# Kernel tuning notes

Hardware: AMD Instinct MI355X
Metric: run time of the kernel (lower is better)

## Reference

```python
import jax, jax.numpy as jnp
import numpy as np


def _conv1x1(t, W, b):
    # 1x1 conv == per-pixel channel GEMM: [B,C,H,W] x [O,C] -> [B,O,H,W]
    return jnp.einsum('bchw,oc->bohw', t, W) + b[None, :, None, None]


def setup_inputs() -> dict:
    key = jax.random.key(0)
    ks = jax.random.split(key, 10)
    B, C, H, W = 8, 256, 96, 96
    s = 1.0 / np.sqrt(C)
    inp = {
        'x': jax.random.normal(ks[0], (B, C, H, W), dtype=jnp.float32),
        'Wq': jax.random.normal(ks[1], (C, C), dtype=jnp.float32) * s,
        'bq': jax.random.normal(ks[2], (C,), dtype=jnp.float32) * 0.01,
        'Wk': jax.random.normal(ks[3], (C, C), dtype=jnp.float32) * s,
        'bk': jax.random.normal(ks[4], (C,), dtype=jnp.float32) * 0.01,
        'Wv': jax.random.normal(ks[5], (C, C), dtype=jnp.float32) * s,
        'bv': jax.random.normal(ks[6], (C,), dtype=jnp.float32) * 0.01,
        'Ws': jax.random.normal(ks[7], (C, C), dtype=jnp.float32) * s,
        'bs': jax.random.normal(ks[8], (C,), dtype=jnp.float32) * 0.01,
        # torch init is zeros; use a nonzero scalar so the attention branch matters
        'gamma': jax.random.normal(ks[9], (1,), dtype=jnp.float32) * 0.5,
    }
    return inp


def reference(x, Wq, bq, Wk, bk, Wv, bv, Ws, bs, gamma):
    B, C, H, W = x.shape
    N = H * W
    # query: [B, N, C]
    q = _conv1x1(x, Wq, bq).reshape(B, C, N).transpose(0, 2, 1)
    # key: 1x1 conv, then stride-3 1x1 conv (== subsample every 3rd pixel, then GEMM)
    k = _conv1x1(x, Wk, bk)
    k = _conv1x1(k[:, :, ::3, ::3], Ws, bs)
    Ns = k.shape[2] * k.shape[3]
    k = k.reshape(B, C, Ns)
    energy = jnp.einsum('bnc,bcm->bnm', q, k)       # [B, N, Ns]
    attn = jax.nn.softmax(energy, axis=-1)
    # value: same 1x1 conv + strided 1x1 conv pipeline
    v = _conv1x1(x, Wv, bv)
    v = _conv1x1(v[:, :, ::3, ::3], Ws, bs).reshape(B, C, Ns)
    out = jnp.einsum('bcm,bnm->bcn', v, attn).reshape(B, C, H, W)
    return gamma[0] * out + x
```

## Files before the change

### kernel.cpp

```cpp
#include <hip/hip_runtime.h>

typedef _Float16 f16;
typedef _Float16 f16x8 __attribute__((ext_vector_type(8)));
typedef __fp16 fp16x2 __attribute__((ext_vector_type(2)));
typedef float f32x4 __attribute__((ext_vector_type(4)));
typedef float f32x16 __attribute__((ext_vector_type(16)));

#define CDIM 256
#define NPIX 9216
#define NB 8

__device__ __forceinline__ f32x4 mfma16(f16x8 a, f16x8 b, f32x4 c) {
  return __builtin_amdgcn_mfma_f32_16x16x32_f16(a, b, c, 0, 0, 0);
}
__device__ __forceinline__ f32x16 mfma32(f16x8 a, f16x8 b, f32x16 c) {
  return __builtin_amdgcn_mfma_f32_32x32x16_f16(a, b, c, 0, 0, 0);
}
__device__ __forceinline__ f16x8 ld8(const f16* p) { return *(const f16x8*)p; }

__device__ __forceinline__ void stage16(const void* g, void* l) {
  __builtin_amdgcn_global_load_lds((const __attribute__((address_space(1))) unsigned int*)g,
                                   (__attribute__((address_space(3))) unsigned int*)l, 16, 0, 0);
}
#define S_BARRIER() do { asm volatile("" ::: "memory"); __builtin_amdgcn_s_barrier(); asm volatile("" ::: "memory"); } while (0)
#define WAIT_VM(N) do { asm volatile("s_waitcnt vmcnt(" #N ")" ::: "memory"); __builtin_amdgcn_sched_barrier(0); } while (0)

__device__ __forceinline__ unsigned pkrtz(float a, float b) {
  union { fp16x2 h; unsigned u; } cv;
  cv.h = __builtin_amdgcn_cvt_pkrtz(a, b);
  return cv.u;
}
union U8 { f16x8 v; unsigned u[4]; };

__device__ __forceinline__ f16x8 pack_swap(float v0, float v1, float v2, float v3,
                                           float v4, float v5, float v6, float v7,
                                           int hh) {
  unsigned a  = pkrtz(v0, v1);
  unsigned b2 = pkrtz(v2, v3);
  unsigned c2 = pkrtz(v4, v5);
  unsigned d2 = pkrtz(v6, v7);
  unsigned ex1 = __shfl_xor(hh ? a : c2, 32);
  unsigned ex2 = __shfl_xor(hh ? b2 : d2, 32);
  U8 r;
  r.u[0] = hh ? ex1 : a;
  r.u[1] = hh ? ex2 : b2;
  r.u[2] = hh ? c2 : ex1;
  r.u[3] = hh ? d2 : ex2;
  return r.v;
}


__global__ void prep_weights(const float* __restrict__ Wq,
                             const float* __restrict__ Wk, const float* __restrict__ bk,
                             const float* __restrict__ Wv, const float* __restrict__ bv,
                             const float* __restrict__ Ws, const float* __restrict__ bs,
                             f16* __restrict__ WqF, f16* __restrict__ Wk2H, f16* __restrict__ Wv2H,
                             float* __restrict__ bk2, float* __restrict__ bv2) {
  int o = blockIdx.x, c = threadIdx.x;
  float ak = 0.f, av = 0.f;
  for (int i = 0; i < CDIM; ++i) {
    float w = Ws[o*CDIM + i];
    ak += w * Wk[i*CDIM + c];
    av += w * Wv[i*CDIM + c];
  }
  Wk2H[o*CDIM + c] = (f16)ak;
  Wv2H[o*CDIM + c] = (f16)av;
  {
    size_t byte = (size_t)((o >> 5)*16 + (c >> 4))*1024
                + (size_t)(((c >> 3) & 1)*32 + (o & 31))*16 + (c & 7)*2;
    *(f16*)((char*)WqF + byte) = (f16)Wq[o*CDIM + c];
  }
  if (c == 0) {
    float sk = 0.f, sv = 0.f;
    for (int i = 0; i < CDIM; ++i) { float w = Ws[o*CDIM + i]; sk += w*bk[i]; sv += w*bv[i]; }
    bk2[o] = sk + bs[o];
    bv2[o] = sv + bs[o];
  }
}

__global__ void transpose_x(const float* __restrict__ x, char* __restrict__ xT) {
  __shared__ f16 tile[32][34];
  int c0 = blockIdx.x * 32, n0 = blockIdx.y * 32, b = blockIdx.z;
  int tx = threadIdx.x, ty = threadIdx.y;
#pragma unroll
  for (int j = 0; j < 4; ++j) {
    int cl = ty + 8*j;
    tile[cl][tx] = (f16)x[(size_t)(b*CDIM + c0 + cl)*NPIX + n0 + tx];
  }
  __syncthreads();
  int tid = ty*32 + tx;
  if (tid < 128) {
    int nl = tid >> 2, u = tid & 3;
    int n = n0 + nl;
    int cu = (c0 >> 3) + u;
    f16x8 v;
#pragma unroll
    for (int e = 0; e < 8; ++e) v[e] = tile[8*u + e][nl];
    size_t byte = (size_t)(b*NPIX + n)*512 + (size_t)((cu ^ (n & 7)) << 4);
    *(f16x8*)(xT + byte) = v;
  }
}

__global__ __launch_bounds__(256) void compute_kv(
    const char* __restrict__ xT, const f16* __restrict__ Wk2H, const f16* __restrict__ Wv2H,
    const float* __restrict__ bk2, const float* __restrict__ bv2,
    char* __restrict__ kB, char* __restrict__ vB) {
  int ch = blockIdx.x;
  int m0 = ch * 32;
  int b = blockIdx.y;
  int tid = threadIdx.x;
  int w = tid >> 6, lane = tid & 63, l15 = lane & 15, q = lane >> 4;
  size_t chbase = (size_t)(b*32 + ch)*16384;

  const char* xrow[2]; int xn7[2];
#pragma unroll
  for (int mt2 = 0; mt2 < 2; ++mt2) {
    int m = m0 + 16*mt2 + l15;
    int n = 288*(m >> 5) + 3*(m & 31);
    xrow[mt2] = xT + (size_t)(b*NPIX + n)*512;
    xn7[mt2] = n & 7;
  }
  const f16 *kwb[4], *vwb[4];
#pragma unroll
  for (int t = 0; t < 4; ++t) {
    kwb[t] = Wk2H + (size_t)(64*w + 16*t + l15)*CDIM + 8*q;
    vwb[t] = Wv2H + (size_t)(64*w + 16*t + l15)*CDIM + 8*q;
  }
  f32x4 accK[2][4] = {};
  f32x4 accV[4][2] = {};
  for (int ks = 0; ks < 8; ++ks) {
    f16x8 am[2], wk[4], wv[4];
#pragma unroll
    for (int mt2 = 0; mt2 < 2; ++mt2)
      am[mt2] = *(const f16x8*)(xrow[mt2] + (((q + 4*ks) ^ xn7[mt2]) << 4));
#pragma unroll
    for (int t = 0; t < 4; ++t) { wk[t] = ld8(kwb[t] + 32*ks); wv[t] = ld8(vwb[t] + 32*ks); }
#pragma unroll
    for (int mt2 = 0; mt2 < 2; ++mt2)
#pragma unroll
      for (int ot = 0; ot < 4; ++ot) {
        accK[mt2][ot] = mfma16(am[mt2], wk[ot], accK[mt2][ot]);
        accV[ot][mt2] = mfma16(wv[ot], am[mt2], accV[ot][mt2]);
      }
  }
#pragma unroll
  for (int mt2 = 0; mt2 < 2; ++mt2)
#pragma unroll
    for (int ot = 0; ot < 4; ++ot) {
      int cin = 64*w + 16*ot + l15;
      float bo = bk2[cin];
      size_t fb = chbase + (size_t)(cin >> 4)*1024 + (size_t)(((cin >> 3) & 1)*32)*16 + (cin & 7)*2;
#pragma unroll
      for (int r = 0; r < 4; ++r) {
        int keyrel = 16*mt2 + 4*q + r;
        *(f16*)(kB + fb + (size_t)keyrel*16) = (f16)(accK[mt2][ot][r] + bo);
      }
    }
#pragma unroll
  for (int ct = 0; ct < 4; ++ct) {
    f32x4 bv4 = *(const f32x4*)(bv2 + 64*w + 16*ct + 4*q);
#pragma unroll
    for (int mt2 = 0; mt2 < 2; ++mt2) {
#pragma unroll
      for (int r = 0; r < 4; ++r) {
        int c = 64*w + 16*ct + 4*q + r;
        size_t byte = chbase + (size_t)(2*(c >> 5) + mt2)*1024
                    + (size_t)((l15 >> 3)*32 + (c & 31))*16 + (l15 & 7)*2;
        *(f16*)(vB + byte) = (f16)(accV[ct][mt2][r] + bv4[r]);
      }
    }
  }
}

__global__ __launch_bounds__(256, 2) void attention(
    const char* __restrict__ xT, const f16* __restrict__ WqF, const float* __restrict__ bq,
    const char* __restrict__ kB, const char* __restrict__ vB,
    const float* __restrict__ xg, const float* __restrict__ gamma_p,
    float* __restrict__ out) {
  __shared__ char lds[65536];

  int bid = blockIdx.x;
  int b = bid & 7;
  int tile = bid >> 3;
  int tid = threadIdx.x;
  int w = tid >> 6, lane = tid & 63, l31 = lane & 31, hh = lane >> 5;
  int n0w = tile*128 + w*32;
  int lane16 = lane * 16;

  const char* kBb = kB + (size_t)b*524288;
  const char* vBb = vB + (size_t)b*524288;

  {
    int so = tid * 16;
#pragma unroll
    for (int r = 0; r < 4; ++r) stage16(kBb + so + r*4096, lds + so + r*4096);
#pragma unroll
    for (int r = 0; r < 4; ++r) stage16(vBb + so + r*4096, lds + 16384 + so + r*4096);
  }

  f16x8 qf[16];
  {
    f16x8 xb[16];
    int n = n0w + l31;
    const char* xrow = xT + (size_t)(b*NPIX + n)*512;
    int n7 = n & 7;
#pragma unroll
    for (int s = 0; s < 16; ++s)
      xb[s] = *(const f16x8*)(xrow + (((2*s + hh) ^ n7) << 4));
#pragma unroll
    for (int ot = 0; ot < 8; ++ot) {
      f32x16 acc;
#pragma unroll
      for (int j = 0; j < 16; ++j) acc[j] = 0.f;
#pragma unroll
      for (int s = 0; s < 16; ++s) {
        f16x8 wa = *(const f16x8*)((const char*)WqF + (size_t)(ot*16 + s)*1024 + lane16);
        acc = mfma32(wa, xb[s], acc);
      }
#pragma unroll
      for (int i = 0; i < 4; ++i) {
        f32x4 bv4 = *(const f32x4*)(bq + 32*ot + 8*i + 4*hh);
#pragma unroll
        for (int j2 = 0; j2 < 4; ++j2) acc[4*i + j2] += bv4[j2];
      }
      qf[2*ot + 0] = pack_swap(acc[0], acc[1], acc[2], acc[3],
                               acc[4], acc[5], acc[6], acc[7], hh);
      qf[2*ot + 1] = pack_swap(acc[8], acc[9], acc[10], acc[11],
                               acc[12], acc[13], acc[14], acc[15], hh);
    }
  }

  f32x16 O[8];
#pragma unroll
  for (int i = 0; i < 8; ++i)
#pragma unroll
    for (int j = 0; j < 16; ++j) O[i][j] = 0.f;
  float m_run = -3e38f, l_run = 0.f;

  for (int t = 0; t < 32; ++t) {
    char* curb = lds + ((t & 1) << 15);
    if (t < 31) {
      const char* ksrc = kBb + (size_t)(t + 1)*16384;
      const char* vsrc = vBb + (size_t)(t + 1)*16384;
      char* kd = lds + (((t + 1) & 1) << 15);
      int so = tid * 16;
#pragma unroll
      for (int r = 0; r < 4; ++r) stage16(ksrc + so + r*4096, kd + so + r*4096);
#pragma unroll
      for (int r = 0; r < 4; ++r) stage16(vsrc + so + r*4096, kd + 16384 + so + r*4096);
      WAIT_VM(8);
    } else {
      WAIT_VM(0);
    }
    S_BARRIER();

    f32x16 S16;
#pragma unroll
    for (int j = 0; j < 16; ++j) S16[j] = 0.f;
    __builtin_amdgcn_s_setprio(1);
#pragma unroll
    for (int s = 0; s < 16; ++s) {
      f16x8 kf = *(const f16x8*)(curb + s*1024 + lane16);
      S16 = mfma32(kf, qf[s], S16);
    }
    __builtin_amdgcn_s_setprio(0);

    float mx = S16[0];
#pragma unroll
    for (int j = 1; j < 16; ++j) mx = fmaxf(mx, S16[j]);
    mx = fmaxf(mx, __shfl_xor(mx, 32));
    if (!__all(mx <= m_run + 8.0f)) {
      float mn = fmaxf(m_run, mx);
      float al = __expf(m_run - mn);
      m_run = mn;
      l_run *= al;
#pragma unroll
      for (int i = 0; i < 8; ++i)
#pragma unroll
        for (int j = 0; j < 16; ++j) O[i][j] *= al;
    }
    float p[16];
    float ls = 0.f;
#pragma unroll
    for (int j = 0; j < 16; ++j) { p[j] = __expf(S16[j] - m_run); ls += p[j]; }
    l_run += ls;

    f16x8 pf0 = pack_swap(p[0], p[1], p[2], p[3], p[4], p[5], p[6], p[7], hh);
    f16x8 pf1 = pack_swap(p[8], p[9], p[10], p[11], p[12], p[13], p[14], p[15], hh);

    __builtin_amdgcn_s_setprio(1);
#pragma unroll
    for (int ct = 0; ct < 8; ++ct) {
      f16x8 vf0 = *(const f16x8*)(curb + 16384 + (ct*2 + 0)*1024 + lane16);
      O[ct] = mfma32(vf0, pf0, O[ct]);
      f16x8 vf1 = *(const f16x8*)(curb + 16384 + (ct*2 + 1)*1024 + lane16);
      O[ct] = mfma32(vf1, pf1, O[ct]);
    }
    __builtin_amdgcn_s_setprio(0);
    S_BARRIER();
  }

  l_run += __shfl_xor(l_run, 32);
  float inv = 1.0f / l_run;
  float g = gamma_p[0];
  int n = n0w + l31;
#pragma unroll
  for (int ct = 0; ct < 8; ++ct)
#pragma unroll
    for (int j = 0; j < 16; ++j) {
      int c = 32*ct + (j & 3) + 8*(j >> 2) + 4*hh;
      size_t idx = (size_t)(b*CDIM + c)*NPIX + n;
      out[idx] = g * (O[ct][j] * inv) + xg[idx];
    }
}

extern "C" void kernel_launch(void* const* d_in, const int* in_sizes, int n_in,
                              void* d_out, int out_size, void* d_ws, size_t ws_size,
                              hipStream_t stream) {
  (void)in_sizes; (void)n_in; (void)out_size; (void)ws_size;
  const float* x     = (const float*)d_in[0];
  const float* Wq    = (const float*)d_in[1];
  const float* bq    = (const float*)d_in[2];
  const float* Wk    = (const float*)d_in[3];
  const float* bk    = (const float*)d_in[4];
  const float* Wv    = (const float*)d_in[5];
  const float* bv    = (const float*)d_in[6];
  const float* Ws    = (const float*)d_in[7];
  const float* bs    = (const float*)d_in[8];
  const float* gamma = (const float*)d_in[9];

  char* ws = (char*)d_ws;
  float* bk2 = (float*)(ws);
  float* bv2 = (float*)(ws + 1024);
  char* xT   = ws + 4096;
  char* kB   = ws + 4096 + 37748736;
  char* vB   = kB + 4194304;
  f16* WqF   = (f16*)(vB + 4194304);
  f16* Wk2H  = WqF + 65536;
  f16* Wv2H  = Wk2H + 65536;

  prep_weights<<<256, 256, 0, stream>>>(Wq, Wk, bk, Wv, bv, Ws, bs, WqF, Wk2H, Wv2H, bk2, bv2);
  transpose_x<<<dim3(8, 288, 8), dim3(32, 8), 0, stream>>>(x, xT);
  compute_kv<<<dim3(32, 8), 256, 0, stream>>>(xT, Wk2H, Wv2H, bk2, bv2, kB, vB);
  attention<<<576, 256, 0, stream>>>(xT, WqF, bq, kB, vB, x, gamma, (float*)d_out);
}
```

Baseline: 197.2 us.

## Split attention warps into QK/softmax producers and PV consumers

Each block now handles 64 query pixels instead of 128. Two waves compute QK^T and the softmax and write the fp16 probabilities and rescale factors to LDS. The other two waves, one step behind, run the PV MFMAs and the final store. The grid doubles and K/V staging is offset so K for step t+1 and V for step t are loaded together. The goal is to overlap the softmax math with the PV matrix work, at the cost of extra LDS traffic, more LDS per block (about 73 KB) and half the pixels per block, which doubles the K/V reloads.

```diff
diff --git a/kernel.cpp b/kernel.cpp
--- a/kernel.cpp
+++ b/kernel.cpp
@@ -24,6 +24,7 @@
 }
 #define S_BARRIER() do { asm volatile("" ::: "memory"); __builtin_amdgcn_s_barrier(); asm volatile("" ::: "memory"); } while (0)
 #define WAIT_VM(N) do { asm volatile("s_waitcnt vmcnt(" #N ")" ::: "memory"); __builtin_amdgcn_sched_barrier(0); } while (0)
+#define WAIT_LGKM0() do { asm volatile("s_waitcnt lgkmcnt(0)" ::: "memory"); __builtin_amdgcn_sched_barrier(0); } while (0)
 
 __device__ __forceinline__ unsigned pkrtz(float a, float b) {
   union { fp16x2 h; unsigned u; } cv;
@@ -177,15 +178,22 @@
     const char* __restrict__ kB, const char* __restrict__ vB,
     const float* __restrict__ xg, const float* __restrict__ gamma_p,
     float* __restrict__ out) {
-  __shared__ char lds[65536];
+  __shared__ char lds[74496];
+  char* ldsK = lds;
+  char* ldsV = lds + 32768;
+  char* ldsP = lds + 65536;
+  float* ldsA = (float*)(lds + 73728);
+  float* ldsL = (float*)(lds + 74240);
 
   int bid = blockIdx.x;
   int b = bid & 7;
   int tile = bid >> 3;
   int tid = threadIdx.x;
   int w = tid >> 6, lane = tid & 63, l31 = lane & 31, hh = lane >> 5;
-  int n0w = tile*128 + w*32;
   int lane16 = lane * 16;
+  bool prod = (w < 2);
+  int rw = prod ? w : (w - 2);
+  int n0w = tile*64 + rw*32;
 
   const char* kBb = kB + (size_t)b*524288;
   const char* vBb = vB + (size_t)b*524288;
@@ -193,13 +201,11 @@
   {
     int so = tid * 16;
 #pragma unroll
-    for (int r = 0; r < 4; ++r) stage16(kBb + so + r*4096, lds + so + r*4096);
-#pragma unroll
-    for (int r = 0; r < 4; ++r) stage16(vBb + so + r*4096, lds + 16384 + so + r*4096);
+    for (int r = 0; r < 4; ++r) stage16(kBb + so + r*4096, ldsK + so + r*4096);
   }
 
   f16x8 qf[16];
-  {
+  if (prod) {
     f16x8 xb[16];
     int n = n0w + l31;
     const char* xrow = xT + (size_t)(b*NPIX + n)*512;
@@ -237,81 +243,122 @@
     for (int j = 0; j < 16; ++j) O[i][j] = 0.f;
   float m_run = -3e38f, l_run = 0.f;
 
-  for (int t = 0; t < 32; ++t) {
-    char* curb = lds + ((t & 1) << 15);
+  for (int t = 0; t <= 32; ++t) {
     if (t < 31) {
+      int so = tid * 16;
       const char* ksrc = kBb + (size_t)(t + 1)*16384;
-      const char* vsrc = vBb + (size_t)(t + 1)*16384;
-      char* kd = lds + (((t + 1) & 1) << 15);
+      char* kd = ldsK + ((t + 1) & 1)*16384;
+#pragma unroll
+      for (int r = 0; r < 4; ++r) stage16(ksrc + so + r*4096, kd + so + r*4096);
+      const char* vsrc = vBb + (size_t)t*16384;
+      char* vd = ldsV + (t & 1)*16384;
+#pragma unroll
+      for (int r = 0; r < 4; ++r) stage16(vsrc + so + r*4096, vd + so + r*4096);
+      WAIT_VM(8);
+    } else if (t == 31) {
       int so = tid * 16;
-#pragma unroll
-      for (int r = 0; r < 4; ++r) stage16(ksrc + so + r*4096, kd + so + r*4096);
-#pragma unroll
-      for (int r = 0; r < 4; ++r) stage16(vsrc + so + r*4096, kd + 16384 + so + r*4096);
-      WAIT_VM(8);
+      const char* vsrc = vBb + (size_t)31*16384;
+      char* vd = ldsV + (31 & 1)*16384;
+#pragma unroll
+      for (int r = 0; r < 4; ++r) stage16(vsrc + so + r*4096, vd + so + r*4096);
+      WAIT_VM(4);
     } else {
       WAIT_VM(0);
     }
     S_BARRIER();
 
-    f32x16 S16;
-#pragma unroll
-    for (int j = 0; j < 16; ++j) S16[j] = 0.f;
-    __builtin_amdgcn_s_setprio(1);
-#pragma unroll
-    for (int s = 0; s < 16; ++s) {
-      f16x8 kf = *(const f16x8*)(curb + s*1024 + lane16);
-      S16 = mfma32(kf, qf[s], S16);
-    }
-    __builtin_amdgcn_s_setprio(0);
-
-    float mx = S16[0];
-#pragma unroll
-    for (int j = 1; j < 16; ++j) mx = fmaxf(mx, S16[j]);
-    mx = fmaxf(mx, __shfl_xor(mx, 32));
-    if (!__all(mx <= m_run + 8.0f)) {
-      float mn = fmaxf(m_run, mx);
-      float al = __expf(m_run - mn);
-      m_run = mn;
-      l_run *= al;
-#pragma unroll
-      for (int i = 0; i < 8; ++i)
-#pragma unroll
-        for (int j = 0; j < 16; ++j) O[i][j] *= al;
-    }
-    float p[16];
-    float ls = 0.f;
-#pragma unroll
-    for (int j = 0; j < 16; ++j) { p[j] = __expf(S16[j] - m_run); ls += p[j]; }
-    l_run += ls;
-
-    f16x8 pf0 = pack_swap(p[0], p[1], p[2], p[3], p[4], p[5], p[6], p[7], hh);
-    f16x8 pf1 = pack_swap(p[8], p[9], p[10], p[11], p[12], p[13], p[14], p[15], hh);
-
-    __builtin_amdgcn_s_setprio(1);
-#pragma unroll
-    for (int ct = 0; ct < 8; ++ct) {
-      f16x8 vf0 = *(const f16x8*)(curb + 16384 + (ct*2 + 0)*1024 + lane16);
-      O[ct] = mfma32(vf0, pf0, O[ct]);
-      f16x8 vf1 = *(const f16x8*)(curb + 16384 + (ct*2 + 1)*1024 + lane16);
-      O[ct] = mfma32(vf1, pf1, O[ct]);
-    }
-    __builtin_amdgcn_s_setprio(0);
+    if (prod && t < 32) {
+      const char* kc = ldsK + (t & 1)*16384;
+      f32x16 SA, SB;
+#pragma unroll
+      for (int j = 0; j < 16; ++j) { SA[j] = 0.f; SB[j] = 0.f; }
+      __builtin_amdgcn_s_setprio(1);
+#pragma unroll
+      for (int s = 0; s < 8; ++s) {
+        f16x8 kfa = *(const f16x8*)(kc + (2*s)*1024 + lane16);
+        SA = mfma32(kfa, qf[2*s], SA);
+        f16x8 kfb = *(const f16x8*)(kc + (2*s + 1)*1024 + lane16);
+        SB = mfma32(kfb, qf[2*s + 1], SB);
+      }
+      __builtin_amdgcn_s_setprio(0);
+      f32x16 S16;
+#pragma unroll
+      for (int j = 0; j < 16; ++j) S16[j] = SA[j] + SB[j];
+
+      float mx = S16[0];
+#pragma unroll
+      for (int j = 1; j < 16; ++j) mx = fmaxf(mx, S16[j]);
+      mx = fmaxf(mx, __shfl_xor(mx, 32));
+      float al = 1.0f;
+      if (!__all(mx <= m_run + 8.0f)) {
+        float mn = fmaxf(m_run, mx);
+        al = __expf(m_run - mn);
+        m_run = mn;
+        l_run *= al;
+      }
+      float ls = 0.f;
+#pragma unroll
+      for (int j = 0; j < 16; ++j) { S16[j] = __expf(S16[j] - m_run); ls += S16[j]; }
+      l_run += ls;
+
+      f16x8 pf0 = pack_swap(S16[0], S16[1], S16[2], S16[3],
+                            S16[4], S16[5], S16[6], S16[7], hh);
+      f16x8 pf1 = pack_swap(S16[8], S16[9], S16[10], S16[11],
+                            S16[12], S16[13], S16[14], S16[15], hh);
+      char* pd = ldsP + (t & 1)*4096 + w*2048;
+      *(f16x8*)(pd + lane16) = pf0;
+      *(f16x8*)(pd + 1024 + lane16) = pf1;
+      if (lane < 32) ldsA[(t & 1)*64 + w*32 + l31] = al;
+    }
+
+    if (!prod && t >= 1) {
+      int tc = t - 1;
+      float al = ldsA[(tc & 1)*64 + rw*32 + l31];
+      if (!__all(al == 1.0f)) {
+#pragma unroll
+        for (int i = 0; i < 8; ++i)
+#pragma unroll
+          for (int j = 0; j < 16; ++j) O[i][j] *= al;
+      }
+      const char* pc = ldsP + (tc & 1)*4096 + rw*2048;
+      f16x8 pf0 = *(const f16x8*)(pc + lane16);
+      f16x8 pf1 = *(const f16x8*)(pc + 1024 + lane16);
+      const char* vc = ldsV + (tc & 1)*16384;
+      __builtin_amdgcn_s_setprio(1);
+#pragma unroll
+      for (int ct = 0; ct < 8; ++ct) {
+        f16x8 vf0 = *(const f16x8*)(vc + (ct*2 + 0)*1024 + lane16);
+        O[ct] = mfma32(vf0, pf0, O[ct]);
+        f16x8 vf1 = *(const f16x8*)(vc + (ct*2 + 1)*1024 + lane16);
+        O[ct] = mfma32(vf1, pf1, O[ct]);
+      }
+      __builtin_amdgcn_s_setprio(0);
+    }
+
+    WAIT_LGKM0();
     S_BARRIER();
   }
 
-  l_run += __shfl_xor(l_run, 32);
-  float inv = 1.0f / l_run;
-  float g = gamma_p[0];
-  int n = n0w + l31;
-#pragma unroll
-  for (int ct = 0; ct < 8; ++ct)
-#pragma unroll
-    for (int j = 0; j < 16; ++j) {
-      int c = 32*ct + (j & 3) + 8*(j >> 2) + 4*hh;
-      size_t idx = (size_t)(b*CDIM + c)*NPIX + n;
-      out[idx] = g * (O[ct][j] * inv) + xg[idx];
-    }
+  if (prod) {
+    float lt = l_run + __shfl_xor(l_run, 32);
+    if (lane < 32) ldsL[w*32 + l31] = lt;
+  }
+  WAIT_LGKM0();
+  S_BARRIER();
+
+  if (!prod) {
+    float inv = 1.0f / ldsL[rw*32 + l31];
+    float g = gamma_p[0];
+    int n = n0w + l31;
+#pragma unroll
+    for (int ct = 0; ct < 8; ++ct)
+#pragma unroll
+      for (int j = 0; j < 16; ++j) {
+        int c = 32*ct + (j & 3) + 8*(j >> 2) + 4*hh;
+        size_t idx = (size_t)(b*CDIM + c)*NPIX + n;
+        out[idx] = g * (O[ct][j] * inv) + xg[idx];
+      }
+  }
 }
 
 extern "C" void kernel_launch(void* const* d_in, const int* in_sizes, int n_in,
@@ -342,5 +389,5 @@
   prep_weights<<<256, 256, 0, stream>>>(Wq, Wk, bk, Wv, bv, Ws, bs, WqF, Wk2H, Wv2H, bk2, bv2);
   transpose_x<<<dim3(8, 288, 8), dim3(32, 8), 0, stream>>>(x, xT);
   compute_kv<<<dim3(32, 8), 256, 0, stream>>>(xT, Wk2H, Wv2H, bk2, bv2, kB, vB);
-  attention<<<576, 256, 0, stream>>>(xT, WqF, bq, kB, vB, x, gamma, (float*)d_out);
-}
+  attention<<<1152, 256, 0, stream>>>(xT, WqF, bq, kB, vB, x, gamma, (float*)d_out);
+}
```

New measurement: 228.8 us. 1.16x slower.
